# Performance work log

Measured on AMD Instinct MI355X. Metric: run time of the kernel, lower is better.

## Reference

```python
import jax, jax.numpy as jnp
import numpy as np

BSZ, D = 64, 65536
N_NODES, N_FEATS, EMBED_DIM = 1024, 256, 256


def setup_inputs() -> dict:
    key = jax.random.key(0)
    k1, k2, k3, k4, k5, k6 = jax.random.split(key, 6)
    flat_inputs = jax.random.normal(k1, (BSZ, D), dtype=jnp.float32)
    node_ids = jax.random.randint(k2, (BSZ, D), 0, N_NODES, dtype=jnp.int64 if jax.config.jax_enable_x64 else jnp.int32)
    feat_ids = jax.random.randint(k3, (BSZ, D), 0, N_FEATS, dtype=jnp.int64 if jax.config.jax_enable_x64 else jnp.int32)
    # Linear(n_feats -> embed_dim): W is (embed_dim, n_feats) like torch, plus bias.
    lim = 1.0 / np.sqrt(N_FEATS)
    W = jax.random.uniform(k4, (EMBED_DIM, N_FEATS), minval=-lim, maxval=lim, dtype=jnp.float32)
    b = jax.random.uniform(k5, (EMBED_DIM,), minval=-lim, maxval=lim, dtype=jnp.float32)
    global_emb = jax.random.normal(k6, (N_NODES, EMBED_DIM), dtype=jnp.float32)
    return {"flat_inputs": flat_inputs, "node_ids": node_ids, "feat_ids": feat_ids,
            "W": W, "b": b, "global_emb": global_emb}


def _expand(vals, node_ids, feat_ids, n_nodes, n_feats):
    # scatter-fill a dense (bsz, n_nodes, n_feats) tensor (zeros elsewhere)
    bsz, d = vals.shape
    batch_ids = jnp.broadcast_to(jnp.arange(bsz)[:, None], (bsz, d))
    out = jnp.zeros((bsz, n_nodes, n_feats), dtype=vals.dtype)
    return out.at[batch_ids.ravel(), node_ids.ravel(), feat_ids.ravel()].set(vals.ravel())


def reference(flat_inputs, node_ids, feat_ids, W, b, global_emb):
    obs_mat = _expand(flat_inputs, node_ids, feat_ids, N_NODES, N_FEATS)
    mask_mat = _expand(jnp.ones_like(flat_inputs), node_ids, feat_ids, N_NODES, N_FEATS)
    obs_counts = mask_mat.sum(-1, keepdims=True)            # (bsz, n_nodes, 1)
    obs_masked = jnp.nan_to_num((obs_mat * mask_mat) / obs_counts)
    missing_node_mask = obs_counts == 0
    # nodewise Linear + global embedding broadcast over batch
    embedded = jnp.einsum('bnf,ef->bne', obs_masked, W) + b + global_emb[None, :, :]
    return embedded, missing_node_mask
```

## Files before the change

### kernel.cpp

```cpp
#include <hip/hip_runtime.h>
#include <hip/hip_bf16.h>

#define BSZ    64
#define DLEN   65536
#define NNODES 1024
#define NFEATS 256
#define EDIM   256
#define NROWS  (BSZ * NNODES)

#define NRANGE  16
#define NBUCKET (BSZ * NRANGE)
#define LCAP    320
#define GCAP    4600
#define WPAD    268

typedef __bf16 bf16x8 __attribute__((ext_vector_type(8)));
typedef float  f32x4  __attribute__((ext_vector_type(4)));

__device__ __forceinline__ unsigned short f2bf(float x) {
  union { float f; unsigned u; } c; c.f = x;
  unsigned r = c.u + 0x7FFFu + ((c.u >> 16) & 1u);
  return (unsigned short)(r >> 16);
}

__global__ __launch_bounds__(512, 8) void bucket_kernel(
    const float* __restrict__ x, const int* __restrict__ nid,
    const int* __restrict__ fid, unsigned* __restrict__ gcnt,
    uint2* __restrict__ gbuf,
    const float* __restrict__ W, unsigned short* __restrict__ Wb) {
  __shared__ uint2 lbuf[NRANGE][LCAP];
  __shared__ unsigned lcnt[NRANGE];
  __shared__ unsigned lbase[NRANGE];

  const int t = threadIdx.x;
  if (t < NRANGE) lcnt[t] = 0;

  if (blockIdx.x < 32) {
    int wi = (blockIdx.x * 512 + t) * 4;
    float4 w = *(const float4*)(W + wi);
    ushort4 o;
    o.x = f2bf(w.x); o.y = f2bf(w.y); o.z = f2bf(w.z); o.w = f2bf(w.w);
    *(ushort4*)(Wb + wi) = o;
  }
  __syncthreads();

  const int b = blockIdx.x >> 4;
  const int base = blockIdx.x * 4096;

#pragma unroll
  for (int k = 0; k < 2; ++k) {
    int i = base + (k * 512 + t) * 4;
    float4 xv = *(const float4*)(x + i);
    int4   nv = *(const int4*)(nid + i);
    int4   fv = *(const int4*)(fid + i);
    int   nd[4] = {nv.x, nv.y, nv.z, nv.w};
    int   ft[4] = {fv.x, fv.y, fv.z, fv.w};
    float vl[4] = {xv.x, xv.y, xv.z, xv.w};
#pragma unroll
    for (int j = 0; j < 4; ++j) {
      int d = (i + j) & 0xFFFF;
      unsigned pack = (((unsigned)(d + 1)) << 15) | ((unsigned)f2bf(vl[j]) >> 1);
      int r = nd[j] >> 6;
      unsigned row = (unsigned)(nd[j] & 63);
      uint2 rec;
      rec.x = pack;
      rec.y = (row << 16) | (row * WPAD + (unsigned)ft[j]);
      unsigned li = atomicAdd(&lcnt[r], 1u);
      if (li < LCAP) {
        lbuf[r][li] = rec;
      } else {
        unsigned gi = atomicAdd(&gcnt[b * NRANGE + r], 1u);
        if (gi < GCAP) gbuf[(size_t)(b * NRANGE + r) * GCAP + gi] = rec;
      }
    }
  }
  __syncthreads();

  if (t < NRANGE) {
    unsigned n = lcnt[t]; if (n > LCAP) n = LCAP;
    lcnt[t] = n;
    lbase[t] = atomicAdd(&gcnt[b * NRANGE + t], n);
  }
  __syncthreads();

  for (int r = 0; r < NRANGE; ++r) {
    unsigned n  = lcnt[r];
    unsigned bs = lbase[r];
    uint2* dst = gbuf + (size_t)(b * NRANGE + r) * GCAP;
    for (unsigned j = t; j < n; j += 512) {
      unsigned gi = bs + j;
      if (gi < GCAP) dst[gi] = lbuf[r][j];
    }
  }
}

__global__ __launch_bounds__(512, 4) void fused_kernel(
    const unsigned* __restrict__ gcnt, const uint2* __restrict__ gbuf,
    const unsigned short* __restrict__ Wb, const float* __restrict__ bias,
    const float* __restrict__ gemb,
    float* __restrict__ out_emb, float* __restrict__ out_mask) {
  __shared__ __align__(16) unsigned win[64 * WPAD];
  __shared__ float scl[64];

  const int t = threadIdx.x;
  const int g = blockIdx.x;
  const int row0 = g * 64;
  const int nb = (g & 15) * 64;

  uint4* wz = (uint4*)win;
  for (int j = t; j < (64 * WPAD) / 4; j += 512) wz[j] = make_uint4(0u, 0u, 0u, 0u);
  __syncthreads();

  int cn = (int)gcnt[g]; if (cn > GCAP) cn = GCAP;
  const uint2* bk = gbuf + (size_t)g * GCAP;
  const uint4* bk4 = (const uint4*)bk;
  int np = cn >> 1;
  {
    uint4 r0, r1, r2, r3, r4;
    bool v0 = t < np, v1 = t + 512 < np, v2 = t + 1024 < np,
         v3 = t + 1536 < np, v4 = t + 2048 < np;
    if (v0) r0 = bk4[t];
    if (v1) r1 = bk4[t + 512];
    if (v2) r2 = bk4[t + 1024];
    if (v3) r3 = bk4[t + 1536];
    if (v4) r4 = bk4[t + 2048];
    if (v0) { atomicMax(&win[r0.y & 0xFFFFu], r0.x); atomicMax(&win[r0.w & 0xFFFFu], r0.z); }
    if (v1) { atomicMax(&win[r1.y & 0xFFFFu], r1.x); atomicMax(&win[r1.w & 0xFFFFu], r1.z); }
    if (v2) { atomicMax(&win[r2.y & 0xFFFFu], r2.x); atomicMax(&win[r2.w & 0xFFFFu], r2.z); }
    if (v3) { atomicMax(&win[r3.y & 0xFFFFu], r3.x); atomicMax(&win[r3.w & 0xFFFFu], r3.z); }
    if (v4) { atomicMax(&win[r4.y & 0xFFFFu], r4.x); atomicMax(&win[r4.w & 0xFFFFu], r4.z); }
    if ((cn & 1) && t == 0) {
      uint2 rec = bk[cn - 1];
      atomicMax(&win[rec.y & 0xFFFFu], rec.x);
    }
  }
  __syncthreads();

  {
    const int lr  = t >> 3;
    const int seg = t & 7;
    const uint4* rowp = (const uint4*)&win[lr * WPAD];
    int c = 0;
#pragma unroll
    for (int j = 0; j < 8; ++j) {
      uint4 w = rowp[seg + 8 * j];
      c += (w.x != 0u) + (w.y != 0u) + (w.z != 0u) + (w.w != 0u);
    }
    c += __shfl_down(c, 4, 8);
    c += __shfl_down(c, 2, 8);
    c += __shfl_down(c, 1, 8);
    if (seg == 0) {
      scl[lr] = c ? 1.0f / (float)c : 0.0f;
      out_mask[row0 + lr] = c ? 0.0f : 1.0f;
    }
  }

  const int wv   = t >> 6;
  const int lane = t & 63;
  const int cl   = lane & 15;
  const int q    = lane >> 4;
  const int col0 = wv * 32;

  f32x4 acc[4][2];
#pragma unroll
  for (int mt = 0; mt < 4; ++mt)
#pragma unroll
    for (int nt = 0; nt < 2; ++nt) acc[mt][nt] = (f32x4)(0.0f);

#pragma unroll
  for (int ks = 0; ks < 8; ++ks) {
    bf16x8 bfr[2];
#pragma unroll
    for (int nt = 0; nt < 2; ++nt) {
      const uint4* wp = (const uint4*)(Wb + (size_t)(col0 + nt * 16 + cl) * NFEATS + ks * 32 + q * 8);
      bfr[nt] = __builtin_bit_cast(bf16x8, *wp);
    }
#pragma unroll
    for (int mt = 0; mt < 4; ++mt) {
      const uint4* ap = (const uint4*)&win[(mt * 16 + cl) * WPAD + ks * 32 + q * 8];
      uint4 lo = ap[0], hi = ap[1];
      uint4 pk;
      pk.x = ((lo.x & 0x7FFFu) << 1) | ((lo.y & 0x7FFFu) << 17);
      pk.y = ((lo.z & 0x7FFFu) << 1) | ((lo.w & 0x7FFFu) << 17);
      pk.z = ((hi.x & 0x7FFFu) << 1) | ((hi.y & 0x7FFFu) << 17);
      pk.w = ((hi.z & 0x7FFFu) << 1) | ((hi.w & 0x7FFFu) << 17);
      bf16x8 afr = __builtin_bit_cast(bf16x8, pk);
#pragma unroll
      for (int nt = 0; nt < 2; ++nt)
        acc[mt][nt] = __builtin_amdgcn_mfma_f32_16x16x32_bf16(afr, bfr[nt], acc[mt][nt], 0, 0, 0);
    }
  }
  __syncthreads();

#pragma unroll
  for (int nt = 0; nt < 2; ++nt) {
    int col = col0 + nt * 16 + cl;
    float bv = bias[col];
#pragma unroll
    for (int mt = 0; mt < 4; ++mt) {
#pragma unroll
      for (int r2 = 0; r2 < 4; ++r2) {
        int row = mt * 16 + q * 4 + r2;
        float o = acc[mt][nt][r2] * scl[row] + bv + gemb[(size_t)(nb + row) * EDIM + col];
        out_emb[(size_t)(row0 + row) * EDIM + col] = o;
      }
    }
  }
}

extern "C" void kernel_launch(void* const* d_in, const int* in_sizes, int n_in,
                              void* d_out, int out_size, void* d_ws, size_t ws_size,
                              hipStream_t stream) {
  const float* x    = (const float*)d_in[0];
  const int*   nid  = (const int*)d_in[1];
  const int*   fid  = (const int*)d_in[2];
  const float* W    = (const float*)d_in[3];
  const float* bias = (const float*)d_in[4];
  const float* gemb = (const float*)d_in[5];

  float* out_emb  = (float*)d_out;
  float* out_mask = out_emb + (size_t)NROWS * EDIM;

  unsigned* gcnt = (unsigned*)d_ws;
  uint2* gbuf = (uint2*)((char*)d_ws + 8192);
  unsigned short* Wb = (unsigned short*)((char*)d_ws + 8192 + (size_t)NBUCKET * GCAP * sizeof(uint2));

  hipMemsetAsync(gcnt, 0, NBUCKET * sizeof(unsigned), stream);
  bucket_kernel<<<(BSZ * DLEN) / 4096, 512, 0, stream>>>(x, nid, fid, gcnt, gbuf, W, Wb);
  fused_kernel<<<NBUCKET, 512, 0, stream>>>(gcnt, gbuf, Wb, bias, gemb, out_emb, out_mask);
}
```

Before: 148.3 us.

## Pre-pack A tile to bf16 in LDS and stage output for coalesced float4 stores

Issues the global bucket loads before zeroing the LDS window so their latency overlaps the zero-fill, and zeroes only the used columns. After counting, each thread repacks its row segment from 32-bit records into compact bf16 pairs in LDS, so the MFMA loop reads one uint4 per fragment with no per-iteration unpacking. The epilogue writes scaled accumulators to LDS, then reads them back as float4 rows and adds bias and global embedding with coalesced 16-byte loads and stores. This adds extra barriers and LDS round trips, and holds more values in registers.

```diff
diff --git a/kernel.cpp b/kernel.cpp
--- a/kernel.cpp
+++ b/kernel.cpp
@@ -13,6 +13,8 @@
 #define LCAP    320
 #define GCAP    4600
 #define WPAD    268
+#define CW      132
+#define TW      260
 
 typedef __bf16 bf16x8 __attribute__((ext_vector_type(8)));
 typedef float  f32x4  __attribute__((ext_vector_type(4)));
@@ -107,44 +109,47 @@
   const int row0 = g * 64;
   const int nb = (g & 15) * 64;
 
-  uint4* wz = (uint4*)win;
-  for (int j = t; j < (64 * WPAD) / 4; j += 512) wz[j] = make_uint4(0u, 0u, 0u, 0u);
-  __syncthreads();
-
   int cn = (int)gcnt[g]; if (cn > GCAP) cn = GCAP;
   const uint2* bk = gbuf + (size_t)g * GCAP;
   const uint4* bk4 = (const uint4*)bk;
   int np = cn >> 1;
+  uint4 r0, r1, r2, r3, r4;
+  bool v0 = t < np, v1 = t + 512 < np, v2 = t + 1024 < np,
+       v3 = t + 1536 < np, v4 = t + 2048 < np;
+  if (v0) r0 = bk4[t];
+  if (v1) r1 = bk4[t + 512];
+  if (v2) r2 = bk4[t + 1024];
+  if (v3) r3 = bk4[t + 1536];
+  if (v4) r4 = bk4[t + 2048];
+
+#pragma unroll
+  for (int k = 0; k < 8; ++k) {
+    int idx = t + k * 512;
+    *(uint4*)&win[(idx >> 6) * WPAD + (idx & 63) * 4] = make_uint4(0u, 0u, 0u, 0u);
+  }
+  __syncthreads();
+
+  if (v0) { atomicMax(&win[r0.y & 0xFFFFu], r0.x); atomicMax(&win[r0.w & 0xFFFFu], r0.z); }
+  if (v1) { atomicMax(&win[r1.y & 0xFFFFu], r1.x); atomicMax(&win[r1.w & 0xFFFFu], r1.z); }
+  if (v2) { atomicMax(&win[r2.y & 0xFFFFu], r2.x); atomicMax(&win[r2.w & 0xFFFFu], r2.z); }
+  if (v3) { atomicMax(&win[r3.y & 0xFFFFu], r3.x); atomicMax(&win[r3.w & 0xFFFFu], r3.z); }
+  if (v4) { atomicMax(&win[r4.y & 0xFFFFu], r4.x); atomicMax(&win[r4.w & 0xFFFFu], r4.z); }
+  if ((cn & 1) && t == 0) {
+    uint2 rec = bk[cn - 1];
+    atomicMax(&win[rec.y & 0xFFFFu], rec.x);
+  }
+  __syncthreads();
+
+  const int lr  = t >> 3;
+  const int seg = t & 7;
+  uint4 rg[8];
   {
-    uint4 r0, r1, r2, r3, r4;
-    bool v0 = t < np, v1 = t + 512 < np, v2 = t + 1024 < np,
-         v3 = t + 1536 < np, v4 = t + 2048 < np;
-    if (v0) r0 = bk4[t];
-    if (v1) r1 = bk4[t + 512];
-    if (v2) r2 = bk4[t + 1024];
-    if (v3) r3 = bk4[t + 1536];
-    if (v4) r4 = bk4[t + 2048];
-    if (v0) { atomicMax(&win[r0.y & 0xFFFFu], r0.x); atomicMax(&win[r0.w & 0xFFFFu], r0.z); }
-    if (v1) { atomicMax(&win[r1.y & 0xFFFFu], r1.x); atomicMax(&win[r1.w & 0xFFFFu], r1.z); }
-    if (v2) { atomicMax(&win[r2.y & 0xFFFFu], r2.x); atomicMax(&win[r2.w & 0xFFFFu], r2.z); }
-    if (v3) { atomicMax(&win[r3.y & 0xFFFFu], r3.x); atomicMax(&win[r3.w & 0xFFFFu], r3.z); }
-    if (v4) { atomicMax(&win[r4.y & 0xFFFFu], r4.x); atomicMax(&win[r4.w & 0xFFFFu], r4.z); }
-    if ((cn & 1) && t == 0) {
-      uint2 rec = bk[cn - 1];
-      atomicMax(&win[rec.y & 0xFFFFu], rec.x);
-    }
-  }
-  __syncthreads();
-
-  {
-    const int lr  = t >> 3;
-    const int seg = t & 7;
     const uint4* rowp = (const uint4*)&win[lr * WPAD];
     int c = 0;
 #pragma unroll
     for (int j = 0; j < 8; ++j) {
-      uint4 w = rowp[seg + 8 * j];
-      c += (w.x != 0u) + (w.y != 0u) + (w.z != 0u) + (w.w != 0u);
+      rg[j] = rowp[seg + 8 * j];
+      c += (rg[j].x != 0u) + (rg[j].y != 0u) + (rg[j].z != 0u) + (rg[j].w != 0u);
     }
     c += __shfl_down(c, 4, 8);
     c += __shfl_down(c, 2, 8);
@@ -154,6 +159,15 @@
       out_mask[row0 + lr] = c ? 0.0f : 1.0f;
     }
   }
+  __syncthreads();
+
+#pragma unroll
+  for (int j = 0; j < 8; ++j) {
+    unsigned w0 = ((rg[j].x & 0x7FFFu) << 1) | ((rg[j].y & 0x7FFFu) << 17);
+    unsigned w1 = ((rg[j].z & 0x7FFFu) << 1) | ((rg[j].w & 0x7FFFu) << 17);
+    *(uint2*)&win[lr * CW + (seg + 8 * j) * 2] = make_uint2(w0, w1);
+  }
+  __syncthreads();
 
   const int wv   = t >> 6;
   const int lane = t & 63;
@@ -177,14 +191,8 @@
     }
 #pragma unroll
     for (int mt = 0; mt < 4; ++mt) {
-      const uint4* ap = (const uint4*)&win[(mt * 16 + cl) * WPAD + ks * 32 + q * 8];
-      uint4 lo = ap[0], hi = ap[1];
-      uint4 pk;
-      pk.x = ((lo.x & 0x7FFFu) << 1) | ((lo.y & 0x7FFFu) << 17);
-      pk.y = ((lo.z & 0x7FFFu) << 1) | ((lo.w & 0x7FFFu) << 17);
-      pk.z = ((hi.x & 0x7FFFu) << 1) | ((hi.y & 0x7FFFu) << 17);
-      pk.w = ((hi.z & 0x7FFFu) << 1) | ((hi.w & 0x7FFFu) << 17);
-      bf16x8 afr = __builtin_bit_cast(bf16x8, pk);
+      bf16x8 afr = __builtin_bit_cast(bf16x8,
+          *(const uint4*)&win[(mt * 16 + cl) * CW + ks * 16 + q * 4]);
 #pragma unroll
       for (int nt = 0; nt < 2; ++nt)
         acc[mt][nt] = __builtin_amdgcn_mfma_f32_16x16x32_bf16(afr, bfr[nt], acc[mt][nt], 0, 0, 0);
@@ -192,18 +200,38 @@
   }
   __syncthreads();
 
-#pragma unroll
-  for (int nt = 0; nt < 2; ++nt) {
-    int col = col0 + nt * 16 + cl;
-    float bv = bias[col];
-#pragma unroll
-    for (int mt = 0; mt < 4; ++mt) {
-#pragma unroll
-      for (int r2 = 0; r2 < 4; ++r2) {
-        int row = mt * 16 + q * 4 + r2;
-        float o = acc[mt][nt][r2] * scl[row] + bv + gemb[(size_t)(nb + row) * EDIM + col];
-        out_emb[(size_t)(row0 + row) * EDIM + col] = o;
+  {
+    float* winf = (float*)win;
+#pragma unroll
+    for (int nt = 0; nt < 2; ++nt) {
+      int col = col0 + nt * 16 + cl;
+#pragma unroll
+      for (int mt = 0; mt < 4; ++mt) {
+#pragma unroll
+        for (int r2 = 0; r2 < 4; ++r2) {
+          int row = mt * 16 + q * 4 + r2;
+          winf[row * TW + col] = acc[mt][nt][r2] * scl[row];
+        }
       }
+    }
+  }
+  __syncthreads();
+
+  {
+    const float* winf = (const float*)win;
+#pragma unroll
+    for (int k = 0; k < 8; ++k) {
+      int f = t + k * 512;
+      int row = f >> 6, cg = (f & 63) * 4;
+      float4 a  = *(const float4*)&winf[row * TW + cg];
+      float4 gv = *(const float4*)&gemb[(size_t)(nb + row) * EDIM + cg];
+      float4 bv = *(const float4*)&bias[cg];
+      float4 o;
+      o.x = a.x + bv.x + gv.x;
+      o.y = a.y + bv.y + gv.y;
+      o.z = a.z + bv.z + gv.z;
+      o.w = a.w + bv.w + gv.w;
+      *(float4*)&out_emb[(size_t)(row0 + row) * EDIM + cg] = o;
     }
   }
 }
```

Measured after the change: 150.5 us. No clear change (+1.5%).
